# Kernel tuning notes

Measured on AMD Instinct MI355X. Metric: run time of the kernel, lower is better.

The kernel has to match this reference:

```python
import jax, jax.numpy as jnp
import numpy as np

PCH_SIZE = 8
STRIDE = 3


def setup_inputs() -> dict:
    key = jax.random.key(0)
    x = jax.random.normal(key, (8, 3, 512, 512), dtype=jnp.float32)
    return {"x": x}


def _estimate_noise(x, p=PCH_SIZE, s=STRIDE):
    B = x.shape[0]
    # Extract overlapping patches: [B, C*p*p, Hp, Wp] (NCHW input).
    pch = jax.lax.conv_general_dilated_patches(x, (p, p), (s, s), 'VALID')
    d = pch.shape[1]                       # C*p*p = 192
    pch = pch.reshape(B, d, -1)            # [B, d, num_pch]
    num_pch = pch.shape[-1]
    mu = pch.mean(axis=-1, keepdims=True)
    X = pch - mu
    # Patch covariance: [B, d, d]
    sigma_X = jnp.einsum('bdn,ben->bde', X, X) / num_pch
    sig = jnp.sort(jnp.linalg.eigvalsh(sigma_X), axis=-1)  # [B, d], ascending

    # Vectorized version of the original sequential threshold search.
    # Loop iteration ii = -1..-d uses prefix sig[..., :d+ii] of length L = d-1..0.
    ks = jnp.arange(d)
    L = d - 1 - ks                          # prefix lengths in original loop order
    csum = jnp.cumsum(sig, axis=-1)         # [B, d]
    prefix_sum = jnp.where(L > 0, csum[:, jnp.clip(L - 1, 0, d - 1)], 0.0)  # [B, d]
    tau = prefix_sum / jnp.maximum(L, 1).astype(sig.dtype)                  # [B, d]

    j = jnp.arange(d)
    in_prefix = j[None, :] < L[:, None]     # [K, d] membership of eig j in prefix k
    greater = (sig[:, None, :] > tau[:, :, None]) & in_prefix[None]
    less = (sig[:, None, :] < tau[:, :, None]) & in_prefix[None]
    valid = greater.sum(axis=-1) == less.sum(axis=-1)  # [B, K]

    # First valid iteration in loop order (mirrors the `found` flag).
    idx = jnp.argmax(valid, axis=-1)                    # [B]
    tau_sel = jnp.take_along_axis(tau, idx[:, None], axis=-1)[:, 0]
    return jnp.sqrt(tau_sel)                             # [B]


def reference(x):
    return _estimate_noise(x)
```

## Files before the change

### kernel.cpp

```cpp
#include <hip/hip_runtime.h>
#include <math.h>

#define NB 8
#define NC 3
#define PD 192
#define IMG 512
#define NP 169
#define NPATCH 28561
#define INV_N (1.0f/28561.0f)
#define KST 32

typedef float f4 __attribute__((ext_vector_type(4)));
typedef __bf16 bf16x8 __attribute__((ext_vector_type(8)));
typedef float f32x4 __attribute__((ext_vector_type(4)));

__device__ __forceinline__ float rdlane(float v, int lane) {
  return __uint_as_float(__builtin_amdgcn_readlane(__float_as_uint(v), lane));
}

template<int CTRL, int RM, int BM>
__device__ __forceinline__ float dpp_add(float x) {
  int sh = __builtin_amdgcn_update_dpp(0, __float_as_int(x), CTRL, RM, BM, false);
  return x + __int_as_float(sh);
}
__device__ __forceinline__ float wave_sum(float x) {
  x = dpp_add<0x111, 0xF, 0xF>(x);
  x = dpp_add<0x112, 0xF, 0xF>(x);
  x = dpp_add<0x114, 0xF, 0xF>(x);
  x = dpp_add<0x118, 0xF, 0xF>(x);
  x = dpp_add<0x142, 0xA, 0xF>(x);
  x = dpp_add<0x143, 0xC, 0xF>(x);
  return rdlane(x, 63);
}
__device__ __forceinline__ float row16_sum(float x) {
  x = dpp_add<0x111, 0xF, 0xF>(x);
  x = dpp_add<0x112, 0xF, 0xF>(x);
  x = dpp_add<0x114, 0xF, 0xF>(x);
  x = dpp_add<0x118, 0xF, 0xF>(x);
  return rdlane(x, 15);
}

__device__ __forceinline__ unsigned bfh(float v) {
  unsigned u = __float_as_uint(v);
  return (u + 0x7FFFu + ((u >> 16) & 1u)) >> 16;
}

__global__ __launch_bounds__(512) void cov_gemm_k(const float* __restrict__ x,
                                                  float* __restrict__ partial,
                                                  float* __restrict__ Spart,
                                                  int CH, int chunkSize) {
  int chunk = blockIdx.x % CH;
  int b = blockIdx.x / CH;
  int p0 = chunk * chunkSize;
  int pcount = NPATCH - p0;
  if (pcount > chunkSize) pcount = chunkSize;
  if (pcount < 0) pcount = 0;
  int nkt = (pcount + KST - 1) / KST;
  int pend = p0 + pcount;

  __shared__ unsigned short hiT[PD * 40];
  __shared__ unsigned short loT[PD * 40];
  __shared__ float sred[PD * 16];

  int t = threadIdx.x;
  int l = t & 63, w = t >> 6;
  int wr = w >> 2, wc = w & 3;
  int m0 = wr * 96, n0 = wc * 48;
  const float* imgb = x + (size_t)b * NC * IMG * IMG;

  f32x4 acc[6][3];
#pragma unroll
  for (int i = 0; i < 6; ++i)
#pragma unroll
    for (int j = 0; j < 3; ++j)
      acc[i][j] = (f32x4){0.f, 0.f, 0.f, 0.f};

  float fsum[6] = {0.f, 0.f, 0.f, 0.f, 0.f, 0.f};

  int krow = (l >> 4) << 3;
  int rsel = l & 15;

  for (int kt = 0; kt < nkt; ++kt) {
    int pbase = p0 + kt * KST;
#pragma unroll
    for (int s = 0; s < 6; ++s) {
      int idx = (s << 9) + t;
      int f = idx >> 4, p2 = idx & 15;
      int c = f >> 6, ii = (f >> 3) & 7, jj = f & 7;
      const float* imgc = imgb + (size_t)c * IMG * IMG;
      int P0 = pbase + (p2 << 1);
      float v0 = 0.f, v1 = 0.f;
      if (P0 < pend) { int ph = P0 / NP, pw = P0 - ph * NP; v0 = imgc[(3 * ph + ii) * IMG + 3 * pw + jj]; }
      if (P0 + 1 < pend) { int ph = (P0 + 1) / NP, pw = (P0 + 1) - ph * NP; v1 = imgc[(3 * ph + ii) * IMG + 3 * pw + jj]; }
      fsum[s] += v0 + v1;
      unsigned h0 = bfh(v0), h1 = bfh(v1);
      float r0 = v0 - __uint_as_float(h0 << 16);
      float r1 = v1 - __uint_as_float(h1 << 16);
      unsigned g0 = bfh(r0), g1 = bfh(r1);
      *(unsigned*)&hiT[f * 40 + (p2 << 1)] = h0 | (h1 << 16);
      *(unsigned*)&loT[f * 40 + (p2 << 1)] = g0 | (g1 << 16);
    }
    __syncthreads();

    bf16x8 ah[6], al[6], bh[3], bl[3];
#pragma unroll
    for (int i = 0; i < 6; ++i) {
      int row = m0 + i * 16 + rsel;
      ah[i] = *(const bf16x8*)&hiT[row * 40 + krow];
      al[i] = *(const bf16x8*)&loT[row * 40 + krow];
    }
#pragma unroll
    for (int j = 0; j < 3; ++j) {
      int row = n0 + j * 16 + rsel;
      bh[j] = *(const bf16x8*)&hiT[row * 40 + krow];
      bl[j] = *(const bf16x8*)&loT[row * 40 + krow];
    }
#pragma unroll
    for (int i = 0; i < 6; ++i)
#pragma unroll
      for (int j = 0; j < 3; ++j) {
        acc[i][j] = __builtin_amdgcn_mfma_f32_16x16x32_bf16(ah[i], bh[j], acc[i][j], 0, 0, 0);
        acc[i][j] = __builtin_amdgcn_mfma_f32_16x16x32_bf16(ah[i], bl[j], acc[i][j], 0, 0, 0);
        acc[i][j] = __builtin_amdgcn_mfma_f32_16x16x32_bf16(al[i], bh[j], acc[i][j], 0, 0, 0);
      }
    __syncthreads();
  }

#pragma unroll
  for (int s = 0; s < 6; ++s) {
    int f = (t >> 4) + (s << 5);
    sred[(f << 4) | (t & 15)] = fsum[s];
  }
  __syncthreads();
  if (t < PD) {
    float s = 0.f;
#pragma unroll
    for (int p2 = 0; p2 < 16; ++p2) s += sred[(t << 4) | p2];
    Spart[((size_t)chunk * NB + b) * PD + t] = s;
  }

  float* outp = partial + ((size_t)chunk * NB + b) * PD * PD;
#pragma unroll
  for (int i = 0; i < 6; ++i) {
    int rowb = m0 + i * 16 + ((l >> 4) << 2);
#pragma unroll
    for (int r = 0; r < 4; ++r)
#pragma unroll
      for (int j = 0; j < 3; ++j)
        outp[(size_t)(rowb + r) * PD + n0 + j * 16 + (l & 15)] = acc[i][j][r];
  }
}

__global__ __launch_bounds__(192) void musum_k(const float* __restrict__ Spart,
                                               float* __restrict__ S, int CH) {
  int b = blockIdx.x, t = threadIdx.x;
  float s = 0.f;
  for (int c = 0; c < CH; ++c) s += Spart[((size_t)c * NB + b) * PD + t];
  S[b * PD + t] = s;
}

__global__ __launch_bounds__(256) void reduce_fin_k(const float* __restrict__ partial,
                                                    const float* __restrict__ S,
                                                    float* __restrict__ G, int CH) {
  int e = blockIdx.x * 256 + threadIdx.x;
  const int tot = NB * PD * PD;
  if (e >= tot) return;
  int b = e / (PD * PD);
  int rem = e - b * PD * PD;
  int i = rem / PD, j = rem - i * PD;
  float s = 0.f;
  for (int c = 0; c < CH; ++c) s += partial[((size_t)c * NB + b) * PD * PD + rem];
  float mui = S[b * PD + i] * INV_N, muj = S[b * PD + j] * INV_N;
  G[e] = s * INV_N - mui * muj;
}

__global__ __launch_bounds__(768, 3) void eigen_k(const float* __restrict__ sigma,
                                                  float* __restrict__ out) {
  __shared__ float ppt[PD][20];
  __shared__ float vvg[2][PD];
  __shared__ float wvg[PD];
  __shared__ float red0[2];
  __shared__ float red2[16];
  __shared__ float dd[PD], ee[PD], e2[PD];
  __shared__ float sig[PD], csum[PD];
  __shared__ float grd[8];
  __shared__ float scanw[4];
  __shared__ int   redi[4];
  __shared__ int   cntb[4][PD];

  int b = blockIdx.x, t = threadIdx.x;
  int w = t >> 6, l = t & 63;
  int colbase = w << 4;
  const float* M = sigma + (size_t)b * PD * PD;

  f4 a[3][4];
#pragma unroll
  for (int rr = 0; rr < 3; ++rr) {
    const float* mp = M + (size_t)((rr << 6) + l) * PD + colbase;
#pragma unroll
    for (int cc = 0; cc < 4; ++cc)
      a[rr][cc] = *(const f4*)(mp + (cc << 2));
  }
  if (t >= 12 && t < 16) red2[t] = 0.f;

  int swc = w + (l >> 3);
  if (swc >= 12) swc -= 12;

  auto extract = [&](int c, float* av) {
#pragma unroll
    for (int cc = 0; cc < 4; ++cc)
#pragma unroll
      for (int e = 0; e < 4; ++e)
        if (colbase + (cc << 2) + e == c) {
          av[0] = a[0][cc][e]; av[1] = a[1][cc][e]; av[2] = a[2][cc][e];
        }
  };

  auto prep_core = [&](int c, float av0, float av1, float av2) {
    int k1 = c + 1;
    float am0 = (l >= k1) ? av0 : 0.f;
    float am1 = (l + 64 >= k1) ? av1 : 0.f;
    float am2 = (l + 128 >= k1) ? av2 : 0.f;
    float sq = wave_sum(am0 * am0 + am1 * am1 + am2 * am2);
    int slot2 = k1 >> 6;
    float tmp = (slot2 == 0) ? av0 : (slot2 == 1) ? av1 : av2;
    float x0 = rdlane(tmp, k1 & 63);
    float nrm = __builtin_amdgcn_sqrtf(sq);
    float alpha = (x0 >= 0.f) ? -nrm : nrm;
    bool degen = (sq < 1e-32f);
    float beta = degen ? 0.f : __builtin_amdgcn_rcpf(sq - alpha * x0);
    if (l == 0) {
      red0[c & 1] = beta;
      ee[c] = degen ? x0 : alpha;
    }
    float head = x0 - alpha;
    vvg[c & 1][l]       = (l       < k1) ? 0.f : (l       == k1) ? head : am0;
    vvg[c & 1][l + 64]  = (l + 64  < k1) ? 0.f : (l + 64  == k1) ? head : am1;
    vvg[c & 1][l + 128] = (l + 128 < k1) ? 0.f : (l + 128 == k1) ? head : am2;
  };

  if (w == 0) {
    float av[3] = {0.f, 0.f, 0.f};
    extract(0, av);
    prep_core(0, av[0], av[1], av[2]);
  }
  __syncthreads();

  for (int k = 0; k < PD - 2; ++k) {
    int cur = k & 1;
    int k1 = k + 1;
    bool wact = (colbase + 15) >= k1;

    float vr[3] = {0.f, 0.f, 0.f};
    f4 sv4[4];

    if (wact) {
      vr[0] = vvg[cur][l]; vr[1] = vvg[cur][l + 64]; vr[2] = vvg[cur][l + 128];
#pragma unroll
      for (int cc = 0; cc < 4; ++cc)
        sv4[cc] = *(const f4*)&vvg[cur][colbase + (cc << 2)];
      float dp = 0.f;
#pragma unroll
      for (int rr = 0; rr < 3; ++rr) {
        if ((rr << 6) + 63 >= k1) {
          f4 s4 = sv4[0] * a[rr][0] + sv4[1] * a[rr][1]
                + sv4[2] * a[rr][2] + sv4[3] * a[rr][3];
          float s = (s4.x + s4.y) + (s4.z + s4.w);
          ppt[(rr << 6) + l][swc] = s;
          dp += vr[rr] * s;
        }
      }
      float dpt = wave_sum(dp);
      if (l == 0) red2[w] = dpt;
    } else if (k1 == colbase + 16) {
      ppt[l][swc] = 0.f; ppt[l + 64][swc] = 0.f; ppt[l + 128][swc] = 0.f;
      if (l == 0) red2[w] = 0.f;
    }
    __syncthreads();

    if (wact) {
      float rv = red2[l & 15];
      float vt = row16_sum(rv);
      float beta = red0[cur];
      float Kc = 0.5f * beta * beta * vt;
      float wr[3] = {0.f, 0.f, 0.f};
#pragma unroll
      for (int rr = 0; rr < 3; ++rr) {
        if ((rr << 6) + 63 >= k1) {
          int row = (rr << 6) + l;
          f4 q = *(const f4*)&ppt[row][0];
          f4 q1 = *(const f4*)&ppt[row][4];
          f4 q2 = *(const f4*)&ppt[row][8];
          q += q1 + q2;
          float p = (q.x + q.y) + (q.z + q.w);
          wr[rr] = (row >= k1) ? (beta * p - Kc * vr[rr]) : 0.f;
          if (rr == (w >> 2)) {
            if ((l >> 4) == (w & 3))
              wvg[row] = wr[rr];
          }
        }
      }
      int cn = k + 1;
      if (w == (cn >> 4)) {
        float av[3] = {0.f, 0.f, 0.f};
        extract(cn, av);
        float svv = vvg[cur][cn];
        float swv = wvg[cn];
#pragma unroll
        for (int rr = 0; rr < 3; ++rr) av[rr] -= vr[rr] * swv + wr[rr] * svv;
        prep_core(cn, av[0], av[1], av[2]);
      }
      f4 sw4[4];
#pragma unroll
      for (int cc = 0; cc < 4; ++cc)
        sw4[cc] = *(const f4*)&wvg[colbase + (cc << 2)];
#pragma unroll
      for (int rr = 0; rr < 3; ++rr) {
        if ((rr << 6) + 63 >= k1) {
          float vrr = vr[rr], wrr = wr[rr];
#pragma unroll
          for (int cc = 0; cc < 4; ++cc)
            a[rr][cc] -= sw4[cc] * vrr + sv4[cc] * wrr;
        }
      }
    }
    __syncthreads();
  }

#pragma unroll
  for (int rr = 0; rr < 3; ++rr) {
    int row = (rr << 6) + l;
#pragma unroll
    for (int cc = 0; cc < 4; ++cc)
#pragma unroll
      for (int e = 0; e < 4; ++e)
        if (colbase + (cc << 2) + e == row) dd[row] = a[rr][cc][e];
  }
  __syncthreads();

  if (t < PD - 1) e2[t] = ee[t] * ee[t];

  float glo = 1e30f, ghi = -1e30f;
  if (t < PD) {
    float r = 0.f;
    if (t > 0) r += fabsf(ee[t - 1]);
    if (t < PD - 1) r += fabsf(ee[t]);
    glo = dd[t] - r;
    ghi = dd[t] + r;
  }
#pragma unroll
  for (int off = 32; off; off >>= 1) {
    glo = fminf(glo, __shfl_xor(glo, off, 64));
    ghi = fmaxf(ghi, __shfl_xor(ghi, off, 64));
  }
  if (l == 0 && w < 3) { grd[w] = glo; grd[4 + w] = ghi; }
  __syncthreads();
  float gl = fminf(grd[0], fminf(grd[1], grd[2]));
  float gh = fmaxf(grd[4], fmaxf(grd[5], grd[6]));
  float wid = gh - gl;
  gl -= 1e-3f * wid + 1e-20f;
  gh += 1e-3f * wid + 1e-20f;

  {
    int we3 = w - (w / 3) * 3;
    int sub = w / 3;
    int e = (we3 << 6) + l;
    float lo = gl, hi = gh;
    for (int round = 0; round < 8; ++round) {
      float width = hi - lo;
      float xm = lo + width * (0.2f * (float)(sub + 1));
      int cnt = 0;
      float q = 1.0f;
      for (int i = 0; i < PD; ++i) {
        float term = (i > 0) ? e2[i - 1] * __builtin_amdgcn_rcpf(q) : 0.0f;
        q = (dd[i] - xm) - term;
        cnt += (q < 0.f);
        float aq = fabsf(q);
        if (aq < 1e-30f) q = (q < 0.f) ? -1e-30f : 1e-30f;
      }
      cntb[sub][e] = cnt;
      __syncthreads();
      int c0 = cntb[0][e], c1 = cntb[1][e], c2 = cntb[2][e], c3 = cntb[3][e];
      float mA = lo + width * 0.2f, mB = lo + width * 0.4f;
      float mC = lo + width * 0.6f, mD = lo + width * 0.8f;
      float nl = lo, nh = hi;
      if (c0 <= e) nl = mA;
      if (c1 <= e) nl = mB;
      if (c2 <= e) nl = mC;
      if (c3 <= e) nl = mD;
      if (c3 > e) nh = mD;
      if (c2 > e) nh = mC;
      if (c1 > e) nh = mB;
      if (c0 > e) nh = mA;
      lo = nl; hi = nh;
      __syncthreads();
    }
    if (sub == 0) sig[e] = 0.5f * (lo + hi);
  }
  __syncthreads();

  {
    float x = (t < PD) ? sig[t] : 0.f;
    float scn = x;
#pragma unroll
    for (int off = 1; off < 64; off <<= 1) {
      float u = __shfl_up(scn, off, 64);
      if (l >= off) scn += u;
    }
    if (l == 63 && w < 3) scanw[w] = scn;
    __syncthreads();
    if (t < PD) {
      float base = 0.f;
      if (w >= 1) base += scanw[0];
      if (w >= 2) base += scanw[1];
      csum[t] = scn + base;
    }
  }
  __syncthreads();

  float tau = 0.f;
  int vk = 1 << 30;
  if (t < PD) {
    int L = PD - 1 - t;
    tau = (L > 0) ? csum[L - 1] / (float)L : 0.0f;
    int gt = 0, lt2 = 0;
    for (int j = 0; j < L; ++j) {
      float svv = sig[j];
      gt  += (svv > tau);
      lt2 += (svv < tau);
    }
    if (gt == lt2) vk = t;
  }
#pragma unroll
  for (int off = 32; off; off >>= 1) vk = min(vk, __shfl_xor(vk, off, 64));
  if (l == 0 && w < 3) redi[w] = vk;
  __syncthreads();
  if (t == 0) {
    int g = min(redi[0], min(redi[1], redi[2]));
    redi[3] = (g == (1 << 30)) ? 0 : g;
  }
  __syncthreads();
  if (t < PD && t == redi[3]) out[b] = sqrtf(fmaxf(tau, 0.f));
}

extern "C" void kernel_launch(void* const* d_in, const int* in_sizes, int n_in,
                              void* d_out, int out_size, void* d_ws, size_t ws_size,
                              hipStream_t stream) {
  const float* x = (const float*)d_in[0];
  float* out = (float*)d_out;

  size_t gElems = (size_t)NB * PD * PD;
  int CH = 32;
  while (CH > 1 &&
         ws_size < ((size_t)CH + 1) * gElems * 4 + (size_t)NB * PD * 4 +
                   (size_t)CH * NB * PD * 4)
    CH >>= 1;
  float* G = (float*)d_ws;
  float* partial = G + gElems;
  float* S = partial + (size_t)CH * gElems;
  float* Spart = S + (size_t)NB * PD;
  int chunkSize = (NPATCH + CH - 1) / CH;

  cov_gemm_k<<<NB * CH, 512, 0, stream>>>(x, partial, Spart, CH, chunkSize);
  musum_k<<<NB, 192, 0, stream>>>(Spart, S, CH);
  reduce_fin_k<<<(int)((gElems + 255) / 256), 256, 0, stream>>>(partial, S, G, CH);
  eigen_k<<<NB, 768, 0, stream>>>(G, out);
}
```

Before: 454.5 us.

## Split eigen kernel into tridiagonalization, multi-block bisection, and final selection kernels

The eigenvalue bisection stage moves out of the single-block-per-batch eigen kernel into its own kernel. Each batch's 192 eigenvalues are spread over 4 blocks, giving 32 blocks instead of 8. A third small kernel then does the prefix scan and threshold selection. The aim is to use more CUs for the Sturm-count bisection. The cost is two extra launches and global round-trips for the diagonal, off-diagonal and eigenvalue arrays. Per-thread sequential work is unchanged, and each CU now holds fewer waves to hide the latency of the dependent reciprocal chain.

```diff
diff --git a/kernel.cpp b/kernel.cpp
--- a/kernel.cpp
+++ b/kernel.cpp
@@ -175,18 +175,14 @@
 }
 
 __global__ __launch_bounds__(768, 3) void eigen_k(const float* __restrict__ sigma,
-                                                  float* __restrict__ out) {
+                                                  float* __restrict__ DDg,
+                                                  float* __restrict__ EEg) {
   __shared__ float ppt[PD][20];
   __shared__ float vvg[2][PD];
   __shared__ float wvg[PD];
   __shared__ float red0[2];
   __shared__ float red2[16];
-  __shared__ float dd[PD], ee[PD], e2[PD];
-  __shared__ float sig[PD], csum[PD];
-  __shared__ float grd[8];
-  __shared__ float scanw[4];
-  __shared__ int   redi[4];
-  __shared__ int   cntb[4][PD];
+  __shared__ float dd[PD], ee[PD];
 
   int b = blockIdx.x, t = threadIdx.x;
   int w = t >> 6, l = t & 63;
@@ -337,14 +333,36 @@
         if (colbase + (cc << 2) + e == row) dd[row] = a[rr][cc][e];
   }
   __syncthreads();
-
-  if (t < PD - 1) e2[t] = ee[t] * ee[t];
+  if (t < PD) {
+    DDg[b * PD + t] = dd[t];
+    EEg[b * PD + t] = (t < PD - 1) ? ee[t] : 0.f;
+  }
+}
+
+__global__ __launch_bounds__(192) void bisect_k(const float* __restrict__ DDg,
+                                                const float* __restrict__ EEg,
+                                                float* __restrict__ SIGg) {
+  __shared__ float dd[PD], e2[PD];
+  __shared__ float grd[8];
+  __shared__ int   cntb[4][48];
+
+  int blk = blockIdx.x;
+  int b = blk >> 2, q = blk & 3;
+  int t = threadIdx.x;
+  int w = t >> 6, l = t & 63;
+
+  float eept = (t < PD) ? EEg[b * PD + t] : 0.f;
+  if (t < PD) {
+    dd[t] = DDg[b * PD + t];
+    e2[t] = eept * eept;
+  }
+  __syncthreads();
 
   float glo = 1e30f, ghi = -1e30f;
-  if (t < PD) {
-    float r = 0.f;
-    if (t > 0) r += fabsf(ee[t - 1]);
-    if (t < PD - 1) r += fabsf(ee[t]);
+  {
+    float r = fabsf(eept);
+    if (t > 0) r += sqrtf(e2[t - 1]);
+    if (t == PD - 1) r = sqrtf(e2[PD - 2]);
     glo = dd[t] - r;
     ghi = dd[t] + r;
   }
@@ -353,7 +371,7 @@
     glo = fminf(glo, __shfl_xor(glo, off, 64));
     ghi = fmaxf(ghi, __shfl_xor(ghi, off, 64));
   }
-  if (l == 0 && w < 3) { grd[w] = glo; grd[4 + w] = ghi; }
+  if (l == 0) { grd[w] = glo; grd[4 + w] = ghi; }
   __syncthreads();
   float gl = fminf(grd[0], fminf(grd[1], grd[2]));
   float gh = fmaxf(grd[4], fmaxf(grd[5], grd[6]));
@@ -361,66 +379,73 @@
   gl -= 1e-3f * wid + 1e-20f;
   gh += 1e-3f * wid + 1e-20f;
 
+  int sub = t / 48;
+  int el = t - sub * 48;
+  int e = q * 48 + el;
+  float lo = gl, hi = gh;
+  for (int round = 0; round < 8; ++round) {
+    float width = hi - lo;
+    float xm = lo + width * (0.2f * (float)(sub + 1));
+    int cnt = 0;
+    float qq = 1.0f;
+    for (int i = 0; i < PD; ++i) {
+      float term = (i > 0) ? e2[i - 1] * __builtin_amdgcn_rcpf(qq) : 0.0f;
+      qq = (dd[i] - xm) - term;
+      cnt += (qq < 0.f);
+      float aq = fabsf(qq);
+      if (aq < 1e-30f) qq = (qq < 0.f) ? -1e-30f : 1e-30f;
+    }
+    cntb[sub][el] = cnt;
+    __syncthreads();
+    int c0 = cntb[0][el], c1 = cntb[1][el], c2 = cntb[2][el], c3 = cntb[3][el];
+    float mA = lo + width * 0.2f, mB = lo + width * 0.4f;
+    float mC = lo + width * 0.6f, mD = lo + width * 0.8f;
+    float nl = lo, nh = hi;
+    if (c0 <= e) nl = mA;
+    if (c1 <= e) nl = mB;
+    if (c2 <= e) nl = mC;
+    if (c3 <= e) nl = mD;
+    if (c3 > e) nh = mD;
+    if (c2 > e) nh = mC;
+    if (c1 > e) nh = mB;
+    if (c0 > e) nh = mA;
+    lo = nl; hi = nh;
+    __syncthreads();
+  }
+  if (sub == 0) SIGg[b * PD + e] = 0.5f * (lo + hi);
+}
+
+__global__ __launch_bounds__(192) void final_k(const float* __restrict__ SIGg,
+                                               float* __restrict__ out) {
+  __shared__ float sig[PD], csum[PD];
+  __shared__ float scanw[4];
+  __shared__ int   redi[4];
+
+  int b = blockIdx.x, t = threadIdx.x;
+  int w = t >> 6, l = t & 63;
+
+  sig[t] = SIGg[b * PD + t];
+  __syncthreads();
+
   {
-    int we3 = w - (w / 3) * 3;
-    int sub = w / 3;
-    int e = (we3 << 6) + l;
-    float lo = gl, hi = gh;
-    for (int round = 0; round < 8; ++round) {
-      float width = hi - lo;
-      float xm = lo + width * (0.2f * (float)(sub + 1));
-      int cnt = 0;
-      float q = 1.0f;
-      for (int i = 0; i < PD; ++i) {
-        float term = (i > 0) ? e2[i - 1] * __builtin_amdgcn_rcpf(q) : 0.0f;
-        q = (dd[i] - xm) - term;
-        cnt += (q < 0.f);
-        float aq = fabsf(q);
-        if (aq < 1e-30f) q = (q < 0.f) ? -1e-30f : 1e-30f;
-      }
-      cntb[sub][e] = cnt;
-      __syncthreads();
-      int c0 = cntb[0][e], c1 = cntb[1][e], c2 = cntb[2][e], c3 = cntb[3][e];
-      float mA = lo + width * 0.2f, mB = lo + width * 0.4f;
-      float mC = lo + width * 0.6f, mD = lo + width * 0.8f;
-      float nl = lo, nh = hi;
-      if (c0 <= e) nl = mA;
-      if (c1 <= e) nl = mB;
-      if (c2 <= e) nl = mC;
-      if (c3 <= e) nl = mD;
-      if (c3 > e) nh = mD;
-      if (c2 > e) nh = mC;
-      if (c1 > e) nh = mB;
-      if (c0 > e) nh = mA;
-      lo = nl; hi = nh;
-      __syncthreads();
-    }
-    if (sub == 0) sig[e] = 0.5f * (lo + hi);
-  }
-  __syncthreads();
-
-  {
-    float x = (t < PD) ? sig[t] : 0.f;
-    float scn = x;
+    float scn = sig[t];
 #pragma unroll
     for (int off = 1; off < 64; off <<= 1) {
       float u = __shfl_up(scn, off, 64);
       if (l >= off) scn += u;
     }
-    if (l == 63 && w < 3) scanw[w] = scn;
-    __syncthreads();
-    if (t < PD) {
-      float base = 0.f;
-      if (w >= 1) base += scanw[0];
-      if (w >= 2) base += scanw[1];
-      csum[t] = scn + base;
-    }
+    if (l == 63) scanw[w] = scn;
+    __syncthreads();
+    float base = 0.f;
+    if (w >= 1) base += scanw[0];
+    if (w >= 2) base += scanw[1];
+    csum[t] = scn + base;
   }
   __syncthreads();
 
   float tau = 0.f;
   int vk = 1 << 30;
-  if (t < PD) {
+  {
     int L = PD - 1 - t;
     tau = (L > 0) ? csum[L - 1] / (float)L : 0.0f;
     int gt = 0, lt2 = 0;
@@ -433,14 +458,14 @@
   }
 #pragma unroll
   for (int off = 32; off; off >>= 1) vk = min(vk, __shfl_xor(vk, off, 64));
-  if (l == 0 && w < 3) redi[w] = vk;
+  if (l == 0) redi[w] = vk;
   __syncthreads();
   if (t == 0) {
     int g = min(redi[0], min(redi[1], redi[2]));
     redi[3] = (g == (1 << 30)) ? 0 : g;
   }
   __syncthreads();
-  if (t < PD && t == redi[3]) out[b] = sqrtf(fmaxf(tau, 0.f));
+  if (t == redi[3]) out[b] = sqrtf(fmaxf(tau, 0.f));
 }
 
 extern "C" void kernel_launch(void* const* d_in, const int* in_sizes, int n_in,
@@ -453,16 +478,21 @@
   int CH = 32;
   while (CH > 1 &&
          ws_size < ((size_t)CH + 1) * gElems * 4 + (size_t)NB * PD * 4 +
-                   (size_t)CH * NB * PD * 4)
+                   (size_t)CH * NB * PD * 4 + 3 * (size_t)NB * PD * 4)
     CH >>= 1;
   float* G = (float*)d_ws;
   float* partial = G + gElems;
   float* S = partial + (size_t)CH * gElems;
   float* Spart = S + (size_t)NB * PD;
+  float* DDg = Spart + (size_t)CH * NB * PD;
+  float* EEg = DDg + (size_t)NB * PD;
+  float* SIGg = EEg + (size_t)NB * PD;
   int chunkSize = (NPATCH + CH - 1) / CH;
 
   cov_gemm_k<<<NB * CH, 512, 0, stream>>>(x, partial, Spart, CH, chunkSize);
   musum_k<<<NB, 192, 0, stream>>>(Spart, S, CH);
   reduce_fin_k<<<(int)((gElems + 255) / 256), 256, 0, stream>>>(partial, S, G, CH);
-  eigen_k<<<NB, 768, 0, stream>>>(G, out);
-}
+  eigen_k<<<NB, 768, 0, stream>>>(G, DDg, EEg);
+  bisect_k<<<NB * 4, 192, 0, stream>>>(DDg, EEg, SIGg);
+  final_k<<<NB, 192, 0, stream>>>(SIGg, out);
+}
```

Result: faster. 441.9 us (-2.8%).
